# Kernel tuning notes

Hardware: AMD Instinct MI355X
Metric: run time of the kernel (lower is better)

## Reference

```python
import jax, jax.numpy as jnp
import numpy as np
from jax import lax

B, C, H, G = 128, 512, 14, 20  # batch, channels, feature-map size, num branches

# landmark indices for (point1, point2) of the 10 regions, and y-offset coefficients (x ruler)
_I1 = jnp.array([21, 18, 19, 41, 38, 49, 48, 51, 61, 56])
_I2 = jnp.array([22, 25, 24, 46, 43, 53, 54, 57, 63, 58])
_COEF = jnp.array([-0.5, -1.0 / 3.0, 1.0 / 3.0, 1.0, 0.0, 0.0, 0.0, 0.0, 0.0, 0.5], jnp.float32)


def process_landmarks(y):
    # y: [B,68,2] (x,y) pixel coords -> region_array [B,10,4] = (x1,y1,x2,y2)/16
    xl, yl = y[:, :, 0], y[:, :, 1]
    ruler = jnp.abs(xl[:, 39] - xl[:, 42])            # [B]
    off = ruler[:, None] * _COEF[None, :]             # [B,10]
    region = jnp.stack([xl[:, _I1], yl[:, _I1] + off, xl[:, _I2], yl[:, _I2] + off], axis=-1)
    return region / 16.0


def _crop(xi, cyi, cxi):
    # xi: [C,H,W]; 3x3 window centered at (cyi, cxi)
    z = jnp.asarray(0, cyi.dtype)
    return lax.dynamic_slice(xi, (z, cyi - 1, cxi - 1), (C, 3, 3))


def setup_inputs() -> dict:
    key = jax.random.key(0)
    ks = jax.random.split(key, 4)
    x = jax.random.normal(ks[0], (B, C, H, H), jnp.float32)
    y = jax.random.uniform(ks[1], (B, 68, 2), jnp.float32) * 224.0
    conv_w = jax.random.normal(ks[2], (G * C, C, 3, 3), jnp.float32) * 0.02  # grouped OIHW
    conv_b = jnp.zeros((G * C,), jnp.float32)
    fc_w = jax.random.normal(ks[3], (G, C * 36, 150), jnp.float32) * 0.01
    fc_b = jnp.zeros((G, 150), jnp.float32)
    return {"x": x, "y": y, "conv_w": conv_w, "conv_b": conv_b, "fc_w": fc_w, "fc_b": fc_b}


def reference(x, y, conv_w, conv_b, fc_w, fc_b):
    bsz = x.shape[0]
    pos = jnp.clip(process_landmarks(y).astype(jnp.int32), 1, 12)   # [B,10,4]
    cx = pos[:, :, jnp.array([0, 2])].reshape(bsz, G)               # [B,20] cols
    cy = pos[:, :, jnp.array([1, 3])].reshape(bsz, G)               # [B,20] rows
    crops = jax.vmap(jax.vmap(_crop, in_axes=(None, 0, 0)), in_axes=(0, 0, 0))(x, cy, cx)  # [B,20,C,3,3]
    new_input = crops.reshape(bsz, G * C, 3, 3)
    up = jax.image.resize(new_input, (bsz, G * C, 6, 6), method='bilinear')  # half-pixel, matches torch align_corners=False
    conv = lax.conv_general_dilated(up, conv_w, (1, 1), ((1, 1), (1, 1)),
                                    feature_group_count=G,
                                    dimension_numbers=('NCHW', 'OIHW', 'NCHW'))
    conv = jax.nn.relu(conv + conv_b[None, :, None, None])          # [B, G*C, 6, 6]
    feat = conv.reshape(bsz, G, C * 36)
    fc = jax.nn.relu(jnp.einsum('bgi,gio->bgo', feat, fc_w) + fc_b[None])  # [B,G,150]
    return fc.reshape(bsz, G * 150)
```

## Files before the change

kernel.cpp:

```cpp
#include <hip/hip_runtime.h>
#include <stdint.h>

#define B_  128
#define C_  512
#define G_  20
#define K2  4608
#define FCK 18432

typedef unsigned short u16;
typedef unsigned int   u32;
typedef __attribute__((ext_vector_type(8))) short  short8;
typedef __attribute__((ext_vector_type(4))) short  short4v;
typedef __attribute__((ext_vector_type(4))) float  float4v;

__device__ __forceinline__ u16 f2bf(float f) {
  u32 u = __builtin_bit_cast(u32, f);
  u = (u + 0x7fffu + ((u >> 16) & 1u)) >> 16;
  return (u16)u;
}

__device__ __forceinline__ void load_lds16(const void* g, void* l) {
  __builtin_amdgcn_global_load_lds(
      (const __attribute__((address_space(1))) void*)(uintptr_t)g,
      (__attribute__((address_space(3))) void*)(uint32_t)(uintptr_t)l,
      16, 0, 0);
}

#define BAR() __builtin_amdgcn_s_barrier()

__global__ void k_pos(const float* __restrict__ y, int* __restrict__ cx, int* __restrict__ cy) {
  int b = blockIdx.x * blockDim.x + threadIdx.x;
  if (b >= B_) return;
  const int   I1[10] = {21,18,19,41,38,49,48,51,61,56};
  const int   I2[10] = {22,25,24,46,43,53,54,57,63,58};
  const float CF[10] = {-0.5f, -1.0f/3.0f, 1.0f/3.0f, 1.0f, 0.f,0.f,0.f,0.f,0.f, 0.5f};
  const float* yb = y + b * 136;
  float ruler = fabsf(yb[2*39] - yb[2*42]);
  for (int j = 0; j < 10; ++j) {
    float off = ruler * CF[j];
    float vx1 = yb[2*I1[j]];
    float vy1 = yb[2*I1[j]+1] + off;
    float vx2 = yb[2*I2[j]];
    float vy2 = yb[2*I2[j]+1] + off;
    int px1 = (int)(vx1 * 0.0625f); px1 = min(max(px1,1),12);
    int py1 = (int)(vy1 * 0.0625f); py1 = min(max(py1,1),12);
    int px2 = (int)(vx2 * 0.0625f); px2 = min(max(px2,1),12);
    int py2 = (int)(vy2 * 0.0625f); py2 = min(max(py2,1),12);
    cx[b*20 + 2*j]   = px1;  cx[b*20 + 2*j+1] = px2;
    cy[b*20 + 2*j]   = py1;  cy[b*20 + 2*j+1] = py2;
  }
}

__global__ void __launch_bounds__(256) k_pre(const float* __restrict__ w, u16* __restrict__ wb,
                                             const float* __restrict__ x,
                                             const int* __restrict__ cx, const int* __restrict__ cy,
                                             u16* __restrict__ up3) {
  __shared__ __align__(16) char smraw[4 * 4608 * 2];
  int tid = threadIdx.x;
  if (blockIdx.x < 2560) {
    u16* lds = (u16*)smraw;
    int ob = blockIdx.x * 4;
    const float4* in4 = (const float4*)(w + (size_t)ob * 4608);
    #pragma unroll
    for (int r = 0; r < 18; ++r) {
      int fi = r * 256 + tid;
      float4 v = in4[fi];
      u16 q[4] = { f2bf(v.x), f2bf(v.y), f2bf(v.z), f2bf(v.w) };
      *(short4v*)&lds[fi * 4] = *(short4v*)q;
    }
    __syncthreads();
    #pragma unroll
    for (int r = 0; r < 9; ++r) {
      int wi = r * 256 + tid;
      int ci0 = (wi & 63) * 8;
      int t   = (wi >> 6) % 9;
      int o   = wi / 576;
      u16 vals[8];
      #pragma unroll
      for (int j = 0; j < 8; ++j) vals[j] = lds[o * 4608 + (ci0 + j) * 9 + t];
      *(short8*)(wb + ((size_t)(ob + o)) * K2 + t * 512 + ci0) = *(short8*)vals;
    }
  } else {
    float (*crop)[3][C_] = (float(*)[3][C_])smraw;
    int bg = blockIdx.x - 2560;
    int b = bg / 20, g = bg % 20;
    int X = cx[bg] - 1, Y = cy[bg] - 1;
    const float* xb = x + (size_t)b * (C_*14*14);
    for (int it = 0; it < 6; ++it) {
      int idx = it*256 + tid;
      int r = idx >> 9, ci = idx & 511;
      const float* srow = xb + ci*196 + (Y + r)*14 + X;
      crop[r][0][ci] = srow[0];
      crop[r][1][ci] = srow[1];
      crop[r][2][ci] = srow[2];
    }
    __syncthreads();
    const int   R0[6] = {0,0,0,1,1,1};
    const float WA[6] = {1.f, .75f, .25f, .75f, .25f, 0.f};
    u16* dstbase = up3 + ((size_t)g*B_ + b) * 64 * C_;
    for (int it = 0; it < 16; ++it) {
      int cidx = it*256 + tid;
      int pp = cidx >> 6;
      int c8 = (cidx & 63) * 8;
      int ph = pp >> 3, pw = pp & 7;
      u16 outv[8];
      if (ph == 0 || ph == 7 || pw == 0 || pw == 7) {
        #pragma unroll
        for (int j = 0; j < 8; ++j) outv[j] = 0;
      } else {
        int oh = ph - 1, ow = pw - 1;
        int r0 = R0[oh]; float wy0 = WA[oh], wy1 = 1.f - WA[oh];
        int s0 = R0[ow]; float wx0 = WA[ow], wx1 = 1.f - WA[ow];
        #pragma unroll
        for (int j = 0; j < 8; ++j) {
          int ci = c8 + j;
          float v = wy0*(wx0*crop[r0][s0][ci]   + wx1*crop[r0][s0+1][ci])
                  + wy1*(wx0*crop[r0+1][s0][ci] + wx1*crop[r0+1][s0+1][ci]);
          outv[j] = f2bf(v);
        }
      }
      *(short8*)(dstbase + (size_t)pp*C_ + c8) = *(short8*)outv;
    }
  }
}

__global__ void __launch_bounds__(512, 2) k_conv(const u16* __restrict__ wb,
                                                 const u16* __restrict__ up3,
                                                 const float* __restrict__ conv_b,
                                                 u16* __restrict__ feat) {
  __shared__ __align__(16) u16 As[2 * 256 * 64];
  __shared__ __align__(16) u16 Bs[2 * 256 * 64];
  int bid = blockIdx.x;
  int lid = (bid & 7) * 90 + (bid >> 3);
  int mt = lid & 1;
  int nt = (lid >> 1) % 18;
  int g  = lid / 36;
  int tid = threadIdx.x;
  int lane = tid & 63;
  int w = tid >> 6;
  int wr = w >> 2, wc = w & 3;
  int l15 = lane & 15, l4 = lane >> 4;

  int rl0 = tid >> 3, sl0 = tid & 7;
  const u16* srcA0 = wb + (size_t)(g*512 + mt*256 + rl0) * K2 + (sl0 ^ (rl0 & 7)) * 8;
  const u16* srcB[2][2];
  #pragma unroll
  for (int h = 0; h < 2; ++h)
    #pragma unroll
    for (int j = 0; j < 2; ++j) {
      int rl = j * 64 + rl0;
      int n  = nt * 256 + h * 128 + rl;
      unsigned bb = (unsigned)n / 36u;
      unsigned pix = (unsigned)n % 36u;
      int pixA = (int)(pix / 6u) * 8 + (int)(pix % 6u);
      srcB[h][j] = up3 + (((size_t)g*B_ + bb)*64 + pixA) * C_ + (sl0 ^ (rl0 & 7)) * 8;
    }

  auto stageA = [&](int st, int h) {
    if (st >= 72) return;
    int db = st & 1;
    size_t ko = (size_t)st * 64;
    #pragma unroll
    for (int j = 0; j < 2; ++j)
      load_lds16(srcA0 + (size_t)(h*128 + j*64) * K2 + ko,
                 (char*)As + db*32768 + h*16384 + (j*512 + tid)*16);
  };
  auto stageB = [&](int st, int h) {
    if (st >= 72) return;
    int db = st & 1;
    int t9 = st >> 3;
    size_t ko = (size_t)((t9/3)*8 + (t9%3)) * C_ + (size_t)(st & 7) * 64;
    #pragma unroll
    for (int j = 0; j < 2; ++j)
      load_lds16(srcB[h][j] + ko,
                 (char*)Bs + db*32768 + h*16384 + (j*512 + tid)*16);
  };

  auto ldfrag = [&](const char* base, int row, int kb) -> short8 {
    int cb = (kb*64 + l4*16) ^ ((row & 7) << 4);
    return *(const short8*)(base + row*128 + cb);
  };

  float4v acc[8][4];
  #pragma unroll
  for (int mi = 0; mi < 8; ++mi)
    #pragma unroll
    for (int nj = 0; nj < 4; ++nj) acc[mi][nj] = (float4v){0.f,0.f,0.f,0.f};

  stageB(0,0); stageB(0,1); stageA(0,0); stageA(0,1);
  stageB(1,0); stageB(1,1); stageA(1,0); stageA(1,1);
  asm volatile("s_waitcnt vmcnt(8)" ::: "memory");
  BAR();

  short8 aF[4][2], b01[2][2], b23[2][2];

#define LDA_HALF(BASE, MH)                                        \
  _Pragma("unroll") for (int mi = 0; mi < 4; ++mi)                \
    _Pragma("unroll") for (int kb = 0; kb < 2; ++kb)              \
      aF[mi][kb] = ldfrag(BASE, wr*128 + ((MH)*4 + mi)*16 + l15, kb);
#define LDB_HALF(BASE, NH, DST)                                   \
  _Pragma("unroll") for (int nj = 0; nj < 2; ++nj)                \
    _Pragma("unroll") for (int kb = 0; kb < 2; ++kb)              \
      DST[nj][kb] = ldfrag(BASE, wc*64 + ((NH)*2 + nj)*16 + l15, kb);
#define MFMA_QUAD(BF, QM, QN)                                     \
  __builtin_amdgcn_s_setprio(1);                                  \
  _Pragma("unroll") for (int kb = 0; kb < 2; ++kb)                \
    _Pragma("unroll") for (int mi = 0; mi < 4; ++mi)              \
      _Pragma("unroll") for (int nj = 0; nj < 2; ++nj)            \
        acc[(QM)*4+mi][(QN)*2+nj] = __builtin_amdgcn_mfma_f32_16x16x32_bf16( \
            aF[mi][kb], BF[nj][kb], acc[(QM)*4+mi][(QN)*2+nj], 0, 0, 0);     \
  __builtin_amdgcn_s_setprio(0);

  for (int it = 0; it < 36; ++it) {
    int t0 = 2 * it;
    const char* A0 = (const char*)As;
    const char* B0 = (const char*)Bs;
    const char* A1 = (const char*)As + 32768;
    const char* B1 = (const char*)Bs + 32768;
    LDA_HALF(A0, 0); LDB_HALF(B0, 0, b01);
    BAR(); MFMA_QUAD(b01, 0, 0); BAR();
    LDB_HALF(B0, 1, b23);
    BAR(); MFMA_QUAD(b23, 0, 1); BAR();
    LDA_HALF(A0, 1);
    stageB(t0 + 2, 0);
    BAR(); MFMA_QUAD(b01, 1, 0); BAR();
    stageB(t0 + 2, 1); stageA(t0 + 2, 0);
    BAR(); MFMA_QUAD(b23, 1, 1);
    if (it < 35) { asm volatile("s_waitcnt vmcnt(6)" ::: "memory"); }
    else         { asm volatile("s_waitcnt vmcnt(0)" ::: "memory"); }
    BAR();
    LDA_HALF(A1, 0); LDB_HALF(B1, 0, b01);
    stageA(t0 + 2, 1);
    BAR(); MFMA_QUAD(b01, 0, 0); BAR();
    LDB_HALF(B1, 1, b23);
    BAR(); MFMA_QUAD(b23, 0, 1); BAR();
    LDA_HALF(A1, 1);
    stageB(t0 + 3, 0);
    BAR(); MFMA_QUAD(b01, 1, 0); BAR();
    stageB(t0 + 3, 1); stageA(t0 + 3, 0); stageA(t0 + 3, 1);
    BAR(); MFMA_QUAD(b23, 1, 1);
    asm volatile("s_waitcnt vmcnt(8)" ::: "memory");
    BAR();
  }
#undef LDA_HALF
#undef LDB_HALF
#undef MFMA_QUAD

  float bias[8][4];
  #pragma unroll
  for (int mi = 0; mi < 8; ++mi)
    #pragma unroll
    for (int r = 0; r < 4; ++r)
      bias[mi][r] = conv_b[g*512 + mt*256 + wr*128 + mi*16 + l4*4 + r];
  #pragma unroll
  for (int nj = 0; nj < 4; ++nj) {
    int n = nt*256 + wc*64 + nj*16 + l15;
    unsigned bb = (unsigned)n / 36u;
    unsigned pix = (unsigned)n % 36u;
    size_t base = ((size_t)g*B_ + bb)*FCK + (size_t)pix*512;
    #pragma unroll
    for (int mi = 0; mi < 8; ++mi) {
      int co0 = mt*256 + wr*128 + mi*16 + l4*4;
      u16 q[4];
      #pragma unroll
      for (int r = 0; r < 4; ++r)
        q[r] = f2bf(fmaxf(acc[mi][nj][r] + bias[mi][r], 0.f));
      *(short4v*)(feat + base + co0) = *(short4v*)q;
    }
  }
}

__global__ void __launch_bounds__(256) k_fc(const u16* __restrict__ feat,
                                            const float* __restrict__ fw,
                                            float* __restrict__ accum) {
  __shared__ __align__(16) u16 As[128*64];
  __shared__ __align__(16) u16 Bs[160*64];
  int sp = blockIdx.x;
  int g  = blockIdx.y;
  int tid = threadIdx.x;
  int lane = tid & 63, w = tid >> 6;
  int wr = w >> 1, wc = w & 1;
  int rl = lane >> 3, s = lane & 7;
  int l15 = lane & 15, l4 = lane >> 4;

  const u16* gA[4]; u16* lA[4];
  #pragma unroll
  for (int i = 0; i < 4; ++i) {
    int r = w*32 + i*8 + rl;
    int c = s ^ (r & 7);
    gA[i] = feat + ((size_t)g*B_ + r)*FCK + c*8;
    lA[i] = (u16*)As + (w*32 + i*8) * 64;
  }

  float4v acc[4][5];
  #pragma unroll
  for (int mi = 0; mi < 4; ++mi)
    #pragma unroll
    for (int nj = 0; nj < 5; ++nj) acc[mi][nj] = (float4v){0.f,0.f,0.f,0.f};

  int kbase = sp * 576;
  for (int stp = 0; stp < 9; ++stp) {
    int i0 = kbase + stp * 64;
    int pix = i0 >> 9;
    int cobase = i0 & 511;
    __syncthreads();
    #pragma unroll
    for (int i = 0; i < 4; ++i) load_lds16(gA[i] + i0, lA[i]);
    #pragma unroll
    for (int bit = 0; bit < 5; ++bit) {
      int idx = bit * 256 + tid;
      int il8 = idx / 160;
      int o   = idx - il8 * 160;
      u16 vals[8];
      if (o < 150) {
        const float* src = fw + ((size_t)g * FCK + (size_t)(cobase + il8 * 8) * 36 + pix) * 150 + o;
        #pragma unroll
        for (int j = 0; j < 8; ++j) vals[j] = f2bf(src[(size_t)j * 5400]);
      } else {
        #pragma unroll
        for (int j = 0; j < 8; ++j) vals[j] = 0;
      }
      *(short8*)((char*)Bs + o * 128 + ((il8 ^ (o & 7)) * 16)) = *(short8*)vals;
    }
    __syncthreads();

    short8 a[4][2], bf[5][2];
    #pragma unroll
    for (int kb = 0; kb < 2; ++kb) {
      #pragma unroll
      for (int mi = 0; mi < 4; ++mi) {
        int row = wr*64 + mi*16 + l15;
        int cb  = (kb*64 + l4*16) ^ ((row & 7) << 4);
        a[mi][kb] = *(const short8*)((const char*)As + row*128 + cb);
      }
      #pragma unroll
      for (int nj = 0; nj < 5; ++nj) {
        int row = wc*80 + nj*16 + l15;
        int cb  = (kb*64 + l4*16) ^ ((row & 7) << 4);
        bf[nj][kb] = *(const short8*)((const char*)Bs + row*128 + cb);
      }
    }
    #pragma unroll
    for (int kb = 0; kb < 2; ++kb)
      #pragma unroll
      for (int mi = 0; mi < 4; ++mi)
        #pragma unroll
        for (int nj = 0; nj < 5; ++nj)
          acc[mi][nj] = __builtin_amdgcn_mfma_f32_16x16x32_bf16(
              a[mi][kb], bf[nj][kb], acc[mi][nj], 0, 0, 0);
  }

  #pragma unroll
  for (int mi = 0; mi < 4; ++mi)
    #pragma unroll
    for (int r = 0; r < 4; ++r) {
      int brow = wr*64 + mi*16 + l4*4 + r;
      #pragma unroll
      for (int nj = 0; nj < 5; ++nj) {
        int o = wc*80 + nj*16 + l15;
        atomicAdd(&accum[((size_t)brow*20 + g)*160 + o], acc[mi][nj][r]);
      }
    }
}

__global__ void k_final(const float* __restrict__ accum, const float* __restrict__ fcb,
                        float* __restrict__ out) {
  int idx = blockIdx.x * 256 + threadIdx.x;
  if (idx >= B_*3000) return;
  unsigned b = (unsigned)idx / 3000u;
  unsigned rem = (unsigned)idx % 3000u;
  unsigned g = rem / 150u, o = rem % 150u;
  out[idx] = fmaxf(accum[((size_t)b*20 + g)*160 + o] + fcb[g*150 + o], 0.f);
}

extern "C" void kernel_launch(void* const* d_in, const int* in_sizes, int n_in,
                              void* d_out, int out_size, void* d_ws, size_t ws_size,
                              hipStream_t stream) {
  const float* x      = (const float*)d_in[0];
  const float* y      = (const float*)d_in[1];
  const float* conv_w = (const float*)d_in[2];
  const float* conv_b = (const float*)d_in[3];
  const float* fc_w   = (const float*)d_in[4];
  const float* fc_b   = (const float*)d_in[5];
  float* out = (float*)d_out;

  char* ws = (char*)d_ws;
  size_t off = 0;
  u16* Wb   = (u16*)(ws + off); off += (size_t)10240 * K2 * 2;
  u16* up3  = (u16*)(ws + off); off += (size_t)G_ * B_ * 64 * C_ * 2;
  u16* feat = (u16*)(ws + off); off += (size_t)G_ * B_ * FCK * 2;
  float* accum = (float*)(ws + off); off += (size_t)B_ * G_ * 160 * 4;
  int* cx = (int*)(ws + off); off += B_ * G_ * 4;
  int* cy = (int*)(ws + off); off += B_ * G_ * 4;

  k_pos<<<1, 128, 0, stream>>>(y, cx, cy);
  hipMemsetAsync(accum, 0, (size_t)B_ * G_ * 160 * 4, stream);
  k_pre<<<5120, 256, 0, stream>>>(conv_w, Wb, x, cx, cy, up3);
  k_conv<<<720, 512, 0, stream>>>(Wb, up3, conv_b, feat);
  k_fc<<<dim3(32, 20), 256, 0, stream>>>(feat, fc_w, accum);
  k_final<<<(B_*3000 + 255)/256, 256, 0, stream>>>(accum, fc_b, out);
}
```

Measured before the change: 603.6 us.

## Convert FC weights to bf16 in extra conv-kernel blocks and drop redundant barriers

Adds 1440 extra blocks to the conv launch. Each one transposes and converts a slice of the fp32 FC weights into a bf16 K-contiguous buffer through an LDS tile. The FC kernel then loads B tiles with async global-to-LDS copies instead of doing strided fp32 loads and converting them inline. The aim is to overlap the weight conversion with the conv GEMM and to make the FC weight loads coalesced. Separately, several barriers after the MFMA quads in the conv main loop are removed to cut sync stalls. This relies on the remaining barriers still protecting LDS reuse, and it needs a larger workspace, falling back to the old path when the workspace is too small.

```diff
diff --git a/kernel.cpp b/kernel.cpp
--- a/kernel.cpp
+++ b/kernel.cpp
@@ -127,15 +127,54 @@
 __global__ void __launch_bounds__(512, 2) k_conv(const u16* __restrict__ wb,
                                                  const u16* __restrict__ up3,
                                                  const float* __restrict__ conv_b,
-                                                 u16* __restrict__ feat) {
+                                                 u16* __restrict__ feat,
+                                                 const float* __restrict__ fw,
+                                                 u16* __restrict__ wfcb) {
   __shared__ __align__(16) u16 As[2 * 256 * 64];
   __shared__ __align__(16) u16 Bs[2 * 256 * 64];
   int bid = blockIdx.x;
+  int tid = threadIdx.x;
+
+  if (bid >= 720) {
+    u16* tile = (u16*)As;
+    int cid = bid - 720;
+    int g = cid / 72, ch = cid - g * 72;
+    for (int cc = 0; cc < 4; ++cc) {
+      int c = ch * 256 + cc * 64;
+      int pix = c >> 9, co0 = c & 511;
+      if (cc) __syncthreads();
+      for (int i2 = 0; i2 < 19; ++i2) {
+        int f = i2 * 512 + tid;
+        if (f < 9600) {
+          int q = f / 150, o = f - q * 150;
+          tile[q * 161 + o] =
+              f2bf(fw[((size_t)g * FCK + (size_t)(co0 + q) * 36 + pix) * 150 + o]);
+        }
+      }
+      __syncthreads();
+      for (int i2 = 0; i2 < 3; ++i2) {
+        int wi = i2 * 512 + tid;
+        if (wi < 1280) {
+          int o = wi >> 3, qc = (wi & 7) * 8;
+          u16 vals[8];
+          if (o < 150) {
+            #pragma unroll
+            for (int j = 0; j < 8; ++j) vals[j] = tile[(qc + j) * 161 + o];
+          } else {
+            #pragma unroll
+            for (int j = 0; j < 8; ++j) vals[j] = 0;
+          }
+          *(short8*)(wfcb + ((size_t)(g * 160 + o)) * FCK + c + qc) = *(short8*)vals;
+        }
+      }
+    }
+    return;
+  }
+
   int lid = (bid & 7) * 90 + (bid >> 3);
   int mt = lid & 1;
   int nt = (lid >> 1) % 18;
   int g  = lid / 36;
-  int tid = threadIdx.x;
   int lane = tid & 63;
   int w = tid >> 6;
   int wr = w >> 2, wc = w & 3;
@@ -218,12 +257,12 @@
     const char* A1 = (const char*)As + 32768;
     const char* B1 = (const char*)Bs + 32768;
     LDA_HALF(A0, 0); LDB_HALF(B0, 0, b01);
-    BAR(); MFMA_QUAD(b01, 0, 0); BAR();
+    BAR(); MFMA_QUAD(b01, 0, 0);
     LDB_HALF(B0, 1, b23);
-    BAR(); MFMA_QUAD(b23, 0, 1); BAR();
+    BAR(); MFMA_QUAD(b23, 0, 1);
     LDA_HALF(A0, 1);
     stageB(t0 + 2, 0);
-    BAR(); MFMA_QUAD(b01, 1, 0); BAR();
+    BAR(); MFMA_QUAD(b01, 1, 0);
     stageB(t0 + 2, 1); stageA(t0 + 2, 0);
     BAR(); MFMA_QUAD(b23, 1, 1);
     if (it < 35) { asm volatile("s_waitcnt vmcnt(6)" ::: "memory"); }
@@ -231,14 +270,16 @@
     BAR();
     LDA_HALF(A1, 0); LDB_HALF(B1, 0, b01);
     stageA(t0 + 2, 1);
-    BAR(); MFMA_QUAD(b01, 0, 0); BAR();
+    BAR(); MFMA_QUAD(b01, 0, 0);
     LDB_HALF(B1, 1, b23);
-    BAR(); MFMA_QUAD(b23, 0, 1); BAR();
+    BAR(); MFMA_QUAD(b23, 0, 1);
     LDA_HALF(A1, 1);
     stageB(t0 + 3, 0);
-    BAR(); MFMA_QUAD(b01, 1, 0); BAR();
-    stageB(t0 + 3, 1); stageA(t0 + 3, 0); stageA(t0 + 3, 1);
-    BAR(); MFMA_QUAD(b23, 1, 1);
+    BAR(); MFMA_QUAD(b01, 1, 0);
+    stageB(t0 + 3, 1); stageA(t0 + 3, 0);
+    BAR();
+    stageA(t0 + 3, 1);
+    MFMA_QUAD(b23, 1, 1);
     asm volatile("s_waitcnt vmcnt(8)" ::: "memory");
     BAR();
   }
@@ -272,6 +313,7 @@
 
 __global__ void __launch_bounds__(256) k_fc(const u16* __restrict__ feat,
                                             const float* __restrict__ fw,
+                                            const u16* __restrict__ wfcb,
                                             float* __restrict__ accum) {
   __shared__ __align__(16) u16 As[128*64];
   __shared__ __align__(16) u16 Bs[160*64];
@@ -291,6 +333,15 @@
     gA[i] = feat + ((size_t)g*B_ + r)*FCK + c*8;
     lA[i] = (u16*)As + (w*32 + i*8) * 64;
   }
+  const u16* gB[5]; u16* lB[5];
+  bool useW = (wfcb != nullptr);
+  #pragma unroll
+  for (int i = 0; i < 5; ++i) {
+    int r = w*40 + i*8 + rl;
+    int c = s ^ (r & 7);
+    gB[i] = useW ? (wfcb + ((size_t)(g*160 + r))*FCK + c*8) : nullptr;
+    lB[i] = (u16*)Bs + (w*40 + i*8) * 64;
+  }
 
   float4v acc[4][5];
   #pragma unroll
@@ -301,26 +352,31 @@
   int kbase = sp * 576;
   for (int stp = 0; stp < 9; ++stp) {
     int i0 = kbase + stp * 64;
-    int pix = i0 >> 9;
-    int cobase = i0 & 511;
     __syncthreads();
     #pragma unroll
     for (int i = 0; i < 4; ++i) load_lds16(gA[i] + i0, lA[i]);
-    #pragma unroll
-    for (int bit = 0; bit < 5; ++bit) {
-      int idx = bit * 256 + tid;
-      int il8 = idx / 160;
-      int o   = idx - il8 * 160;
-      u16 vals[8];
-      if (o < 150) {
-        const float* src = fw + ((size_t)g * FCK + (size_t)(cobase + il8 * 8) * 36 + pix) * 150 + o;
-        #pragma unroll
-        for (int j = 0; j < 8; ++j) vals[j] = f2bf(src[(size_t)j * 5400]);
-      } else {
-        #pragma unroll
-        for (int j = 0; j < 8; ++j) vals[j] = 0;
-      }
-      *(short8*)((char*)Bs + o * 128 + ((il8 ^ (o & 7)) * 16)) = *(short8*)vals;
+    if (useW) {
+      #pragma unroll
+      for (int i = 0; i < 5; ++i) load_lds16(gB[i] + i0, lB[i]);
+    } else {
+      int pix = i0 >> 9;
+      int cobase = i0 & 511;
+      #pragma unroll
+      for (int bit = 0; bit < 5; ++bit) {
+        int idx = bit * 256 + tid;
+        int il8 = idx / 160;
+        int o   = idx - il8 * 160;
+        u16 vals[8];
+        if (o < 150) {
+          const float* src = fw + ((size_t)g * FCK + (size_t)(cobase + il8 * 8) * 36 + pix) * 150 + o;
+          #pragma unroll
+          for (int j = 0; j < 8; ++j) vals[j] = f2bf(src[(size_t)j * 5400]);
+        } else {
+          #pragma unroll
+          for (int j = 0; j < 8; ++j) vals[j] = 0;
+        }
+        *(short8*)((char*)Bs + o * 128 + ((il8 ^ (o & 7)) * 16)) = *(short8*)vals;
+      }
     }
     __syncthreads();
 
@@ -392,11 +448,14 @@
   float* accum = (float*)(ws + off); off += (size_t)B_ * G_ * 160 * 4;
   int* cx = (int*)(ws + off); off += B_ * G_ * 4;
   int* cy = (int*)(ws + off); off += B_ * G_ * 4;
+  u16* Wfcb = (u16*)(ws + off); off += (size_t)G_ * 160 * FCK * 2;
+  bool fuse = (ws_size >= off);
 
   k_pos<<<1, 128, 0, stream>>>(y, cx, cy);
   hipMemsetAsync(accum, 0, (size_t)B_ * G_ * 160 * 4, stream);
   k_pre<<<5120, 256, 0, stream>>>(conv_w, Wb, x, cx, cy, up3);
-  k_conv<<<720, 512, 0, stream>>>(Wb, up3, conv_b, feat);
-  k_fc<<<dim3(32, 20), 256, 0, stream>>>(feat, fc_w, accum);
+  k_conv<<<fuse ? 2160 : 720, 512, 0, stream>>>(Wb, up3, conv_b, feat, fc_w,
+                                                fuse ? Wfcb : (u16*)nullptr);
+  k_fc<<<dim3(32, 20), 256, 0, stream>>>(feat, fc_w, fuse ? Wfcb : (u16*)nullptr, accum);
   k_final<<<(B_*3000 + 255)/256, 256, 0, stream>>>(accum, fc_b, out);
 }
```

Result: no change. 607.4 us (+0.6%).

## Transpose input to channel-last bf16 before cropping and trim conv barriers

Applied to the files above, without the earlier changes.

Splits preprocessing into two kernels. The first converts x to a bf16 pixel-major, channel-contiguous layout alongside the weight repack. The second gathers the 3x3 crops with 16-byte vector loads and does the bilinear upsample, replacing the strided per-channel float gathers. Separately, the conv main loop drops the trailing barriers after each MFMA quad and moves one A stage after a barrier. This adds an extra launch and a full pass over x, and relies on the remaining barriers to protect LDS reuse. The input is also rounded to bf16 before interpolation rather than after.

```diff
diff --git a/kernel.cpp b/kernel.cpp
--- a/kernel.cpp
+++ b/kernel.cpp
@@ -17,6 +17,11 @@
   u32 u = __builtin_bit_cast(u32, f);
   u = (u + 0x7fffu + ((u >> 16) & 1u)) >> 16;
   return (u16)u;
+}
+
+__device__ __forceinline__ float bf2f(u16 h) {
+  u32 u = ((u32)h) << 16;
+  return __builtin_bit_cast(float, u);
 }
 
 __device__ __forceinline__ void load_lds16(const void* g, void* l) {
@@ -51,10 +56,8 @@
   }
 }
 
-__global__ void __launch_bounds__(256) k_pre(const float* __restrict__ w, u16* __restrict__ wb,
-                                             const float* __restrict__ x,
-                                             const int* __restrict__ cx, const int* __restrict__ cy,
-                                             u16* __restrict__ up3) {
+__global__ void __launch_bounds__(256) k_pre1(const float* __restrict__ w, u16* __restrict__ wb,
+                                              const float* __restrict__ x, u16* __restrict__ xT) {
   __shared__ __align__(16) char smraw[4 * 4608 * 2];
   int tid = threadIdx.x;
   if (blockIdx.x < 2560) {
@@ -81,46 +84,80 @@
       *(short8*)(wb + ((size_t)(ob + o)) * K2 + t * 512 + ci0) = *(short8*)vals;
     }
   } else {
-    float (*crop)[3][C_] = (float(*)[3][C_])smraw;
-    int bg = blockIdx.x - 2560;
-    int b = bg / 20, g = bg % 20;
-    int X = cx[bg] - 1, Y = cy[bg] - 1;
-    const float* xb = x + (size_t)b * (C_*14*14);
-    for (int it = 0; it < 6; ++it) {
-      int idx = it*256 + tid;
-      int r = idx >> 9, ci = idx & 511;
-      const float* srow = xb + ci*196 + (Y + r)*14 + X;
-      crop[r][0][ci] = srow[0];
-      crop[r][1][ci] = srow[1];
-      crop[r][2][ci] = srow[2];
+    u16* lds = (u16*)smraw;
+    int cid = blockIdx.x - 2560;
+    int b = cid >> 3, cic = (cid & 7) * 64;
+    const float* src = x + ((size_t)b * C_ + cic) * 196;
+    #pragma unroll
+    for (int it = 0; it < 49; ++it) {
+      int idx = it * 256 + tid;
+      int ci = idx / 196, p = idx - ci * 196;
+      lds[ci * 197 + p] = f2bf(src[(size_t)ci * 196 + p]);
     }
     __syncthreads();
-    const int   R0[6] = {0,0,0,1,1,1};
-    const float WA[6] = {1.f, .75f, .25f, .75f, .25f, 0.f};
-    u16* dstbase = up3 + ((size_t)g*B_ + b) * 64 * C_;
-    for (int it = 0; it < 16; ++it) {
-      int cidx = it*256 + tid;
-      int pp = cidx >> 6;
-      int c8 = (cidx & 63) * 8;
-      int ph = pp >> 3, pw = pp & 7;
-      u16 outv[8];
-      if (ph == 0 || ph == 7 || pw == 0 || pw == 7) {
+    u16* dst = xT + (size_t)b * 196 * C_ + cic;
+    #pragma unroll
+    for (int it = 0; it < 7; ++it) {
+      int idx = it * 256 + tid;
+      if (idx < 1568) {
+        int p = idx >> 3, c8 = (idx & 7) * 8;
+        u16 vals[8];
         #pragma unroll
-        for (int j = 0; j < 8; ++j) outv[j] = 0;
-      } else {
-        int oh = ph - 1, ow = pw - 1;
-        int r0 = R0[oh]; float wy0 = WA[oh], wy1 = 1.f - WA[oh];
-        int s0 = R0[ow]; float wx0 = WA[ow], wx1 = 1.f - WA[ow];
-        #pragma unroll
-        for (int j = 0; j < 8; ++j) {
-          int ci = c8 + j;
-          float v = wy0*(wx0*crop[r0][s0][ci]   + wx1*crop[r0][s0+1][ci])
-                  + wy1*(wx0*crop[r0+1][s0][ci] + wx1*crop[r0+1][s0+1][ci]);
-          outv[j] = f2bf(v);
-        }
-      }
-      *(short8*)(dstbase + (size_t)pp*C_ + c8) = *(short8*)outv;
-    }
+        for (int j = 0; j < 8; ++j) vals[j] = lds[(c8 + j) * 197 + p];
+        *(short8*)(dst + (size_t)p * C_ + c8) = *(short8*)vals;
+      }
+    }
+  }
+}
+
+__global__ void __launch_bounds__(256) k_pre2(const u16* __restrict__ xT,
+                                              const int* __restrict__ cx,
+                                              const int* __restrict__ cy,
+                                              u16* __restrict__ up3) {
+  __shared__ float crop[3][3][C_];
+  int bg = blockIdx.x;
+  int b = bg / 20, g = bg % 20;
+  int X = cx[bg] - 1, Y = cy[bg] - 1;
+  int tid = threadIdx.x;
+  const u16* xb = xT + (size_t)b * 196 * C_;
+  #pragma unroll
+  for (int it = 0; it < 3; ++it) {
+    int idx = it * 256 + tid;
+    if (idx < 576) {
+      int pos = idx >> 6;
+      int r = pos / 3, s = pos - r * 3;
+      int c8 = (idx & 63) * 8;
+      short8 v = *(const short8*)(xb + (size_t)((Y + r) * 14 + X + s) * C_ + c8);
+      #pragma unroll
+      for (int j = 0; j < 8; ++j) crop[r][s][c8 + j] = bf2f((u16)v[j]);
+    }
+  }
+  __syncthreads();
+  const int   R0[6] = {0,0,0,1,1,1};
+  const float WA[6] = {1.f, .75f, .25f, .75f, .25f, 0.f};
+  u16* dstbase = up3 + ((size_t)g*B_ + b) * 64 * C_;
+  for (int it = 0; it < 16; ++it) {
+    int cidx = it*256 + tid;
+    int pp = cidx >> 6;
+    int c8 = (cidx & 63) * 8;
+    int ph = pp >> 3, pw = pp & 7;
+    u16 outv[8];
+    if (ph == 0 || ph == 7 || pw == 0 || pw == 7) {
+      #pragma unroll
+      for (int j = 0; j < 8; ++j) outv[j] = 0;
+    } else {
+      int oh = ph - 1, ow = pw - 1;
+      int r0 = R0[oh]; float wy0 = WA[oh], wy1 = 1.f - WA[oh];
+      int s0 = R0[ow]; float wx0 = WA[ow], wx1 = 1.f - WA[ow];
+      #pragma unroll
+      for (int j = 0; j < 8; ++j) {
+        int ci = c8 + j;
+        float v = wy0*(wx0*crop[r0][s0][ci]   + wx1*crop[r0][s0+1][ci])
+                + wy1*(wx0*crop[r0+1][s0][ci] + wx1*crop[r0+1][s0+1][ci]);
+        outv[j] = f2bf(v);
+      }
+    }
+    *(short8*)(dstbase + (size_t)pp*C_ + c8) = *(short8*)outv;
   }
 }
 
@@ -131,11 +168,11 @@
   __shared__ __align__(16) u16 As[2 * 256 * 64];
   __shared__ __align__(16) u16 Bs[2 * 256 * 64];
   int bid = blockIdx.x;
+  int tid = threadIdx.x;
   int lid = (bid & 7) * 90 + (bid >> 3);
   int mt = lid & 1;
   int nt = (lid >> 1) % 18;
   int g  = lid / 36;
-  int tid = threadIdx.x;
   int lane = tid & 63;
   int w = tid >> 6;
   int wr = w >> 2, wc = w & 3;
@@ -218,12 +255,12 @@
     const char* A1 = (const char*)As + 32768;
     const char* B1 = (const char*)Bs + 32768;
     LDA_HALF(A0, 0); LDB_HALF(B0, 0, b01);
-    BAR(); MFMA_QUAD(b01, 0, 0); BAR();
+    BAR(); MFMA_QUAD(b01, 0, 0);
     LDB_HALF(B0, 1, b23);
-    BAR(); MFMA_QUAD(b23, 0, 1); BAR();
+    BAR(); MFMA_QUAD(b23, 0, 1);
     LDA_HALF(A0, 1);
     stageB(t0 + 2, 0);
-    BAR(); MFMA_QUAD(b01, 1, 0); BAR();
+    BAR(); MFMA_QUAD(b01, 1, 0);
     stageB(t0 + 2, 1); stageA(t0 + 2, 0);
     BAR(); MFMA_QUAD(b23, 1, 1);
     if (it < 35) { asm volatile("s_waitcnt vmcnt(6)" ::: "memory"); }
@@ -231,14 +268,16 @@
     BAR();
     LDA_HALF(A1, 0); LDB_HALF(B1, 0, b01);
     stageA(t0 + 2, 1);
-    BAR(); MFMA_QUAD(b01, 0, 0); BAR();
+    BAR(); MFMA_QUAD(b01, 0, 0);
     LDB_HALF(B1, 1, b23);
-    BAR(); MFMA_QUAD(b23, 0, 1); BAR();
+    BAR(); MFMA_QUAD(b23, 0, 1);
     LDA_HALF(A1, 1);
     stageB(t0 + 3, 0);
-    BAR(); MFMA_QUAD(b01, 1, 0); BAR();
-    stageB(t0 + 3, 1); stageA(t0 + 3, 0); stageA(t0 + 3, 1);
-    BAR(); MFMA_QUAD(b23, 1, 1);
+    BAR(); MFMA_QUAD(b01, 1, 0);
+    stageB(t0 + 3, 1); stageA(t0 + 3, 0);
+    BAR();
+    stageA(t0 + 3, 1);
+    MFMA_QUAD(b23, 1, 1);
     asm volatile("s_waitcnt vmcnt(8)" ::: "memory");
     BAR();
   }
@@ -389,13 +428,15 @@
   u16* Wb   = (u16*)(ws + off); off += (size_t)10240 * K2 * 2;
   u16* up3  = (u16*)(ws + off); off += (size_t)G_ * B_ * 64 * C_ * 2;
   u16* feat = (u16*)(ws + off); off += (size_t)G_ * B_ * FCK * 2;
+  u16* xT   = (u16*)(ws + off); off += (size_t)B_ * 196 * C_ * 2;
   float* accum = (float*)(ws + off); off += (size_t)B_ * G_ * 160 * 4;
   int* cx = (int*)(ws + off); off += B_ * G_ * 4;
   int* cy = (int*)(ws + off); off += B_ * G_ * 4;
 
   k_pos<<<1, 128, 0, stream>>>(y, cx, cy);
   hipMemsetAsync(accum, 0, (size_t)B_ * G_ * 160 * 4, stream);
-  k_pre<<<5120, 256, 0, stream>>>(conv_w, Wb, x, cx, cy, up3);
+  k_pre1<<<3584, 256, 0, stream>>>(conv_w, Wb, x, xT);
+  k_pre2<<<B_*G_, 256, 0, stream>>>(xT, cx, cy, up3);
   k_conv<<<720, 512, 0, stream>>>(Wb, up3, conv_b, feat);
   k_fc<<<dim3(32, 20), 256, 0, stream>>>(feat, fc_w, accum);
   k_final<<<(B_*3000 + 255)/256, 256, 0, stream>>>(accum, fc_b, out);
```

Measured after the change: 559.5 us, median of 2. -7.3%, faster.
